# Optimization experiments

Measured on AMD Instinct MI355X. Metric: run time of the kernel, lower is better.

## Reference

```python
import jax, jax.numpy as jnp
import numpy as np

CURRENT_TIME = 1000.0
TIME_WEIGHT = 0.1
NEG_INF = -1e9


def setup_inputs() -> dict:
    key = jax.random.key(0)
    ks = jax.random.split(key, 7)
    B, M, D, C = 1024, 65536, 64, 16
    return {
        "query": jax.random.normal(ks[0], (B, D), dtype=jnp.float32),
        "context": jax.random.normal(ks[1], (B, C), dtype=jnp.float32),
        "mem_keys": jax.random.normal(ks[2], (M, D), dtype=jnp.float32) * 0.1,
        "mem_values": jax.random.normal(ks[3], (M, D), dtype=jnp.float32) * 0.1,
        "mem_contexts": jax.random.normal(ks[4], (M, C), dtype=jnp.float32) * 0.1,
        "mem_timestamps": jax.random.uniform(ks[5], (M, 1), dtype=jnp.float32) * CURRENT_TIME,
        "used_mask": jax.random.randint(ks[6], (M,), 0, 2) > 0,
    }


def reference(query, context, mem_keys, mem_values, mem_contexts, mem_timestamps, used_mask):
    # content score: [B, M]
    scores = jnp.einsum("bd,md->bm", query, mem_keys)
    # context score, scaled by 0.5
    scores = scores + 0.5 * jnp.einsum("bc,mc->bm", context, mem_contexts)
    # time-decay bias, scaled by 0.3 (broadcast over batch)
    decay = jnp.exp(-TIME_WEIGHT * (CURRENT_TIME - mem_timestamps[:, 0]))  # [M]
    scores = scores + 0.3 * decay[None, :]
    # unused slots get -1e9 exactly as torch.full init
    scores = jnp.where(used_mask[None, :], scores, NEG_INF)
    attn = jax.nn.softmax(scores, axis=-1)
    return jnp.einsum("bm,md->bd", attn, mem_values)
```

## Files before the change

### kernel.cpp

```cpp
#include <hip/hip_runtime.h>

typedef float f32x4 __attribute__((ext_vector_type(4)));
typedef __bf16 bf16x8 __attribute__((ext_vector_type(8)));
typedef unsigned int u32;
typedef unsigned short u16;

#define MTOT 65536
#define BTOT 1024
#define DD 64
#define LOG2E 1.44269504088896340736f
#define MFMA __builtin_amdgcn_mfma_f32_16x16x32_bf16

#define NROWBLK ((MTOT + BTOT) * 24 / 256)
#define NVTBLK  (MTOT / 64)
#define ESPACE  (DD * BTOT + BTOT)
#define NSLICE  8

__device__ __forceinline__ u16 f2bf(float f) { return __builtin_bit_cast(u16, (__bf16)f); }
__device__ __forceinline__ u32 pk2(float a, float b) {
    return (u32)f2bf(a) | ((u32)f2bf(b) << 16);
}
__device__ __forceinline__ bf16x8 ldg8(const u16* p) { return *reinterpret_cast<const bf16x8*>(p); }
__device__ __forceinline__ float fexp2(float x) {
#if __has_builtin(__builtin_amdgcn_exp2f)
    return __builtin_amdgcn_exp2f(x);
#else
    return exp2f(x);
#endif
}
__device__ __forceinline__ void glds16(const void* g, void* l) {
    __builtin_amdgcn_global_load_lds((const __attribute__((address_space(1))) u32*)g,
                                     (__attribute__((address_space(3))) u32*)l, 16, 0, 0);
}

__global__ __launch_bounds__(256)
void prep_all(const float* __restrict__ q, const float* __restrict__ ctx,
              const float* __restrict__ K, const float* __restrict__ CT,
              const float* __restrict__ TS, const int* __restrict__ mask,
              const float* __restrict__ V,
              u16* __restrict__ Qc, u16* __restrict__ KC, u16* __restrict__ Vt)
{
    __shared__ u16 L[64][68];
    const int blk = blockIdx.x, t = threadIdx.x;

    if (blk < NROWBLK) {
        const int R = MTOT + BTOT;
        int gid = blk * 256 + t;
        float4 v = {0.f, 0.f, 0.f, 0.f};
        u16* dst;
        if (gid < R * 16) {
            int row = gid >> 4, qd = gid & 15;
            bool isQ = row >= MTOT;
            int r2 = isQ ? row - MTOT : row;
            v = *reinterpret_cast<const float4*>((isQ ? q : K) + (size_t)r2 * 64 + qd * 4);
            if (isQ) { v.x *= LOG2E; v.y *= LOG2E; v.z *= LOG2E; v.w *= LOG2E; }
            dst = (isQ ? Qc : KC) + (size_t)r2 * 96 + qd * 4;
        } else if (gid < R * 20) {
            int i = gid - R * 16;
            int row = i >> 2, qd = i & 3;
            bool isQ = row >= MTOT;
            int r2 = isQ ? row - MTOT : row;
            v = *reinterpret_cast<const float4*>((isQ ? ctx : CT) + (size_t)r2 * 16 + qd * 4);
            if (isQ) { const float s = 0.5f * LOG2E; v.x *= s; v.y *= s; v.z *= s; v.w *= s; }
            dst = (isQ ? Qc : KC) + (size_t)r2 * 96 + 64 + qd * 4;
        } else {
            int i = gid - R * 20;
            int row = i >> 2, qd = i & 3;
            bool isQ = row >= MTOT;
            int r2 = isQ ? row - MTOT : row;
            if (qd == 0)
                v.x = isQ ? LOG2E
                          : (mask[r2] ? 0.3f * __expf(-0.1f * (1000.0f - TS[r2])) : -100.0f);
            dst = (isQ ? Qc : KC) + (size_t)r2 * 96 + 80 + qd * 4;
        }
        ushort4 o = { f2bf(v.x), f2bf(v.y), f2bf(v.z), f2bf(v.w) };
        *reinterpret_cast<ushort4*>(dst) = o;
        return;
    }

    const int m0 = (blk - NROWBLK) * 64;
#pragma unroll
    for (int p = 0; p < 4; ++p) {
        int fi = t + p * 256;
        int mi = fi >> 4, di = (fi & 15) << 2;
        float4 v = *reinterpret_cast<const float4*>(V + (size_t)(m0 + mi) * 64 + di);
        ushort4 o = { f2bf(v.x), f2bf(v.y), f2bf(v.z), f2bf(v.w) };
        *reinterpret_cast<ushort4*>(&L[mi][di]) = o;
    }
    __syncthreads();
    const int d = t >> 2, seg = t & 3;
    u32 pk[8];
#pragma unroll
    for (int pr = 0; pr < 8; ++pr) {
        int c0 = seg * 16 + pr * 2;
        int g32 = c0 >> 5;
        int i0 = c0 & 31, i1 = (c0 + 1) & 31;
        int mp0 = g32 * 32 + (i0 >> 1) + (i0 & 1) * 16;
        int mp1 = g32 * 32 + (i1 >> 1) + (i1 & 1) * 16;
        pk[pr] = (u32)L[mp0][d] | ((u32)L[mp1][d] << 16);
    }
    uint4 A = {pk[0], pk[1], pk[2], pk[3]}, B4 = {pk[4], pk[5], pk[6], pk[7]};
    u16* dst = Vt + (size_t)d * MTOT + m0 + seg * 16;
    *reinterpret_cast<uint4*>(dst)     = A;
    *reinterpret_cast<uint4*>(dst + 8) = B4;
}

__global__ __launch_bounds__(256, 2)
void epmem_mfma(const u16* __restrict__ Qc, const u16* __restrict__ KCg,
                const u16* __restrict__ Vtg,
                float* __restrict__ pl, float* __restrict__ pacc,
                int mper, int NB)
{
    __shared__ __align__(16) u16 KCs[2][64 * 96];
    __shared__ __align__(16) u16 Vts[2][64 * 64];
    __shared__ __align__(16) u16 Pb[4][32][40];

    const int tid = threadIdx.x;
    const int w = tid >> 6, lane = tid & 63;
    const int l15 = lane & 15, g = lane >> 4;

    const int bid = blockIdx.x;
    const int o = (bid & 7) * (NB >> 3) + (bid >> 3);
    const int rt = o & 3, ch = o >> 2;
    const int rbase = rt * 256 + w * 64;

    const u16* qp = Qc + (size_t)(rbase + l15) * 96 + g * 8;
    bf16x8 qf[4][3];
#pragma unroll
    for (int sb = 0; sb < 4; ++sb)
#pragma unroll
        for (int c = 0; c < 3; ++c)
            qf[sb][c] = ldg8(qp + sb * 16 * 96 + c * 32);

    const int m0 = ch * mper;
    const int m1 = (m0 + mper < MTOT) ? (m0 + mper) : MTOT;
    const int ntiles = (m1 > m0) ? ((m1 - m0) >> 6) : 0;

    int kgo[3];
#pragma unroll
    for (int i = 0; i < 3; ++i) {
        int ol = w * 3072 + i * 1024 + lane * 16;
        int row = ol / 192;
        int c = (ol - row * 192) >> 4;
        int u = (c < 8) ? (c ^ (row & 7)) : (8 + ((c & 3) ^ (row & 3)));
        kgo[i] = row * 192 + u * 16;
    }
    int vgo[2];
#pragma unroll
    for (int i = 0; i < 2; ++i) {
        int ol = w * 2048 + i * 1024 + lane * 16;
        int row = ol >> 7, c = (ol >> 4) & 7;
        int u = c ^ (row & 7);
        vgo[i] = row * (MTOT * 2) + u * 16;
    }

    const u32 ow = (l15 == 0) ? 0x3F803F80u : 0u;
    const uint4 ou = {ow, ow, ow, ow};
    const bf16x8 onesf = __builtin_bit_cast(bf16x8, ou);

    f32x4 acc[4][4];
    f32x4 accl[4];
#pragma unroll
    for (int sb = 0; sb < 4; ++sb) {
        accl[sb] = (f32x4){0, 0, 0, 0};
#pragma unroll
        for (int d4 = 0; d4 < 4; ++d4) acc[sb][d4] = (f32x4){0, 0, 0, 0};
    }

    if (ntiles > 0) {
        const char* kb = (const char*)KCg + (size_t)m0 * 192;
        const char* vb = (const char*)Vtg + (size_t)m0 * 2;
#pragma unroll
        for (int i = 0; i < 3; ++i) glds16(kb + kgo[i], (char*)KCs[0] + w * 3072 + i * 1024);
#pragma unroll
        for (int i = 0; i < 2; ++i) glds16(vb + vgo[i], (char*)Vts[0] + w * 2048 + i * 1024);
    }
    __syncthreads();

    char* pbw = (char*)Pb[w];
    const int xr = l15 & 7;
    const int x3 = l15 & 3;

    int cur = 0;
    for (int t = 0; t < ntiles; ++t) {
        if (t + 1 < ntiles) {
            int mt = m0 + ((t + 1) << 6);
            const char* kb = (const char*)KCg + (size_t)mt * 192;
            const char* vb = (const char*)Vtg + (size_t)mt * 2;
            int nb = cur ^ 1;
#pragma unroll
            for (int i = 0; i < 3; ++i) glds16(kb + kgo[i], (char*)KCs[nb] + w * 3072 + i * 1024);
#pragma unroll
            for (int i = 0; i < 2; ++i) glds16(vb + vgo[i], (char*)Vts[nb] + w * 2048 + i * 1024);
        }
        const char* kcb = (const char*)KCs[cur];
        const char* vtb = (const char*)Vts[cur];

#pragma unroll
        for (int j = 0; j < 2; ++j) {
            bf16x8 kf[2][3];
#pragma unroll
            for (int s = 0; s < 2; ++s) {
                int row = j * 32 + s * 16 + l15;
                kf[s][0] = *reinterpret_cast<const bf16x8*>(kcb + row * 192 + (((0 + g) ^ xr) << 4));
                kf[s][1] = *reinterpret_cast<const bf16x8*>(kcb + row * 192 + (((4 + g) ^ xr) << 4));
                kf[s][2] = *reinterpret_cast<const bf16x8*>(kcb + row * 192 + ((8 + (g ^ x3)) << 4));
            }
            bf16x8 vf[4];
#pragma unroll
            for (int d4 = 0; d4 < 4; ++d4) {
                int row = d4 * 16 + l15;
                vf[d4] = *reinterpret_cast<const bf16x8*>(vtb + row * 128 + (((j * 4 + g) ^ xr) << 4));
            }

#pragma unroll
            for (int h = 0; h < 2; ++h) {
                f32x4 S00 = {0,0,0,0}, S01 = {0,0,0,0}, S10 = {0,0,0,0}, S11 = {0,0,0,0};
                S00 = MFMA(qf[2*h][0],   kf[0][0], S00,0,0,0); S00 = MFMA(qf[2*h][1],   kf[0][1], S00,0,0,0); S00 = MFMA(qf[2*h][2],   kf[0][2], S00,0,0,0);
                S01 = MFMA(qf[2*h][0],   kf[1][0], S01,0,0,0); S01 = MFMA(qf[2*h][1],   kf[1][1], S01,0,0,0); S01 = MFMA(qf[2*h][2],   kf[1][2], S01,0,0,0);
                S10 = MFMA(qf[2*h+1][0], kf[0][0], S10,0,0,0); S10 = MFMA(qf[2*h+1][1], kf[0][1], S10,0,0,0); S10 = MFMA(qf[2*h+1][2], kf[0][2], S10,0,0,0);
                S11 = MFMA(qf[2*h+1][0], kf[1][0], S11,0,0,0); S11 = MFMA(qf[2*h+1][1], kf[1][1], S11,0,0,0); S11 = MFMA(qf[2*h+1][2], kf[1][2], S11,0,0,0);

#pragma unroll
                for (int r = 0; r < 4; ++r) {
                    float p00 = fexp2(S00[r]), p01 = fexp2(S01[r]);
                    float p10 = fexp2(S10[r]), p11 = fexp2(S11[r]);
                    int row0 = g * 4 + r, row1 = 16 + g * 4 + r;
                    int cw = (((l15 >> 2) ^ r) << 4) | ((l15 & 3) << 2);
                    *(u32*)(pbw + row0 * 80 + cw) = pk2(p00, p01);
                    *(u32*)(pbw + row1 * 80 + cw) = pk2(p10, p11);
                }
                bf16x8 pa0 = *reinterpret_cast<const bf16x8*>(pbw + l15 * 80        + ((g ^ x3) << 4));
                bf16x8 pa1 = *reinterpret_cast<const bf16x8*>(pbw + (16 + l15) * 80 + ((g ^ x3) << 4));

                acc[2*h][0]   = MFMA(pa0, vf[0], acc[2*h][0],0,0,0);   acc[2*h][1]   = MFMA(pa0, vf[1], acc[2*h][1],0,0,0);
                acc[2*h][2]   = MFMA(pa0, vf[2], acc[2*h][2],0,0,0);   acc[2*h][3]   = MFMA(pa0, vf[3], acc[2*h][3],0,0,0);
                acc[2*h+1][0] = MFMA(pa1, vf[0], acc[2*h+1][0],0,0,0); acc[2*h+1][1] = MFMA(pa1, vf[1], acc[2*h+1][1],0,0,0);
                acc[2*h+1][2] = MFMA(pa1, vf[2], acc[2*h+1][2],0,0,0); acc[2*h+1][3] = MFMA(pa1, vf[3], acc[2*h+1][3],0,0,0);
                accl[2*h]   = MFMA(pa0, onesf, accl[2*h],0,0,0);
                accl[2*h+1] = MFMA(pa1, onesf, accl[2*h+1],0,0,0);
            }
        }
        __syncthreads();
        cur ^= 1;
    }

    if (l15 == 0) {
#pragma unroll
        for (int sb = 0; sb < 4; ++sb)
            *reinterpret_cast<f32x4*>(pl + (size_t)ch * BTOT + rbase + sb * 16 + g * 4) = accl[sb];
    }

    float* bp = pacc + ((size_t)ch * DD + l15) * BTOT + rbase + g * 4;
#pragma unroll
    for (int sb = 0; sb < 4; ++sb)
#pragma unroll
        for (int d4 = 0; d4 < 4; ++d4)
            *reinterpret_cast<f32x4*>(bp + (size_t)(d4 * 16) * BTOT + sb * 16) = acc[sb][d4];
}

__global__ __launch_bounds__(256)
void combineA(const float* __restrict__ pl, const float* __restrict__ pacc,
              float* __restrict__ part, int cper)
{
    int e = blockIdx.x * 256 + threadIdx.x;
    int s = blockIdx.y;
    int c0 = s * cper;
    float v0 = 0.f, v1 = 0.f;
    if (e < DD * BTOT) {
        const float* p = pacc + (size_t)c0 * (DD * BTOT) + e;
#pragma unroll 2
        for (int i = 0; i + 1 < cper; i += 2) {
            v0 += p[(size_t)i * (DD * BTOT)];
            v1 += p[(size_t)(i + 1) * (DD * BTOT)];
        }
        if (cper & 1) v0 += p[(size_t)(cper - 1) * (DD * BTOT)];
    } else {
        const float* p = pl + (size_t)c0 * BTOT + (e - DD * BTOT);
#pragma unroll 2
        for (int i = 0; i + 1 < cper; i += 2) {
            v0 += p[(size_t)i * BTOT];
            v1 += p[(size_t)(i + 1) * BTOT];
        }
        if (cper & 1) v0 += p[(size_t)(cper - 1) * BTOT];
    }
    part[(size_t)s * ESPACE + e] = v0 + v1;
}

__global__ __launch_bounds__(256)
void combineB(const float* __restrict__ part, float* __restrict__ out)
{
    int t = blockIdx.x * 256 + threadIdx.x;
    int d = t >> 10, b = t & 1023;
    float v = 0.f, lssum = 0.f;
#pragma unroll
    for (int s = 0; s < NSLICE; ++s) {
        v     += part[(size_t)s * ESPACE + t];
        lssum += part[(size_t)s * ESPACE + DD * BTOT + b];
    }
    out[(size_t)b * DD + d] = v / lssum;
}

extern "C" void kernel_launch(void* const* d_in, const int* in_sizes, int n_in,
                              void* d_out, int out_size, void* d_ws, size_t ws_size,
                              hipStream_t stream)
{
    const float* q    = (const float*)d_in[0];
    const float* ctx  = (const float*)d_in[1];
    const float* K    = (const float*)d_in[2];
    const float* V    = (const float*)d_in[3];
    const float* CT   = (const float*)d_in[4];
    const float* TS   = (const float*)d_in[5];
    const int*   mask = (const int*)d_in[6];

    char* wsb = (char*)d_ws;
    u16* Qc = (u16*)(wsb);
    u16* KC = (u16*)(wsb + 196608);
    u16* Vt = (u16*)(wsb + 196608 + 12582912);
    size_t fixed = 196608 + 12582912 + 8388608;

    size_t chunk = (size_t)BTOT * (DD + 1) * sizeof(float);
    size_t partB = (size_t)NSLICE * ESPACE * sizeof(float);
    int SPLIT = (int)((ws_size - fixed - partB) / chunk);
    if (SPLIT > 128) SPLIT = 128;
    SPLIT &= ~7;
    if (SPLIT < 8) SPLIT = 8;

    float* pl   = (float*)(wsb + fixed);
    float* pacc = pl + (size_t)SPLIT * BTOT;
    float* part = pacc + (size_t)SPLIT * DD * BTOT;

    int mper = ((MTOT + SPLIT - 1) / SPLIT + 63) & ~63;
    int cper = SPLIT / NSLICE;

    prep_all<<<NROWBLK + NVTBLK, 256, 0, stream>>>(q, ctx, K, CT, TS, mask, V, Qc, KC, Vt);

    int NB = 4 * SPLIT;
    epmem_mfma<<<NB, 256, 0, stream>>>(Qc, KC, Vt, pl, pacc, mper, NB);

    dim3 gA((ESPACE + 255) / 256, NSLICE);
    combineA<<<gA, 256, 0, stream>>>(pl, pacc, part, cper);
    combineB<<<(DD * BTOT) / 256, 256, 0, stream>>>(part, (float*)d_out);
}
```

Measured before the change: 56.01 us.

## Split attention block into eight waves of 32 rows each

The main MFMA kernel now runs 512 threads (8 waves) per block, and each wave handles 32 query rows instead of 64. This halves per-wave query fragments and accumulators, which cuts register pressure and allows higher occupancy (launch bounds 512,4). Only the first four waves issue the async global-to-LDS loads, so the loaded K/V tile is shared by twice as many waves. The cost is more waves contending for LDS reads of K/V fragments, with each wave doing less MFMA work per LDS load.

```diff
diff --git a/kernel.cpp b/kernel.cpp
--- a/kernel.cpp
+++ b/kernel.cpp
@@ -105,7 +105,7 @@
     *reinterpret_cast<uint4*>(dst + 8) = B4;
 }
 
-__global__ __launch_bounds__(256, 2)
+__global__ __launch_bounds__(512, 4)
 void epmem_mfma(const u16* __restrict__ Qc, const u16* __restrict__ KCg,
                 const u16* __restrict__ Vtg,
                 float* __restrict__ pl, float* __restrict__ pacc,
@@ -113,7 +113,7 @@
 {
     __shared__ __align__(16) u16 KCs[2][64 * 96];
     __shared__ __align__(16) u16 Vts[2][64 * 64];
-    __shared__ __align__(16) u16 Pb[4][32][40];
+    __shared__ __align__(16) u16 Pb[8][32][40];
 
     const int tid = threadIdx.x;
     const int w = tid >> 6, lane = tid & 63;
@@ -122,12 +122,12 @@
     const int bid = blockIdx.x;
     const int o = (bid & 7) * (NB >> 3) + (bid >> 3);
     const int rt = o & 3, ch = o >> 2;
-    const int rbase = rt * 256 + w * 64;
+    const int rbase = rt * 256 + w * 32;
 
     const u16* qp = Qc + (size_t)(rbase + l15) * 96 + g * 8;
-    bf16x8 qf[4][3];
-#pragma unroll
-    for (int sb = 0; sb < 4; ++sb)
+    bf16x8 qf[2][3];
+#pragma unroll
+    for (int sb = 0; sb < 2; ++sb)
 #pragma unroll
         for (int c = 0; c < 3; ++c)
             qf[sb][c] = ldg8(qp + sb * 16 * 96 + c * 32);
@@ -136,38 +136,39 @@
     const int m1 = (m0 + mper < MTOT) ? (m0 + mper) : MTOT;
     const int ntiles = (m1 > m0) ? ((m1 - m0) >> 6) : 0;
 
-    int kgo[3];
-#pragma unroll
-    for (int i = 0; i < 3; ++i) {
-        int ol = w * 3072 + i * 1024 + lane * 16;
-        int row = ol / 192;
-        int c = (ol - row * 192) >> 4;
-        int u = (c < 8) ? (c ^ (row & 7)) : (8 + ((c & 3) ^ (row & 3)));
-        kgo[i] = row * 192 + u * 16;
-    }
-    int vgo[2];
-#pragma unroll
-    for (int i = 0; i < 2; ++i) {
-        int ol = w * 2048 + i * 1024 + lane * 16;
-        int row = ol >> 7, c = (ol >> 4) & 7;
-        int u = c ^ (row & 7);
-        vgo[i] = row * (MTOT * 2) + u * 16;
+    int kgo[3], vgo[2];
+    if (w < 4) {
+#pragma unroll
+        for (int i = 0; i < 3; ++i) {
+            int ol = w * 3072 + i * 1024 + lane * 16;
+            int row = ol / 192;
+            int c = (ol - row * 192) >> 4;
+            int u = (c < 8) ? (c ^ (row & 7)) : (8 + ((c & 3) ^ (row & 3)));
+            kgo[i] = row * 192 + u * 16;
+        }
+#pragma unroll
+        for (int i = 0; i < 2; ++i) {
+            int ol = w * 2048 + i * 1024 + lane * 16;
+            int row = ol >> 7, c = (ol >> 4) & 7;
+            int u = c ^ (row & 7);
+            vgo[i] = row * (MTOT * 2) + u * 16;
+        }
     }
 
     const u32 ow = (l15 == 0) ? 0x3F803F80u : 0u;
     const uint4 ou = {ow, ow, ow, ow};
     const bf16x8 onesf = __builtin_bit_cast(bf16x8, ou);
 
-    f32x4 acc[4][4];
-    f32x4 accl[4];
-#pragma unroll
-    for (int sb = 0; sb < 4; ++sb) {
+    f32x4 acc[2][4];
+    f32x4 accl[2];
+#pragma unroll
+    for (int sb = 0; sb < 2; ++sb) {
         accl[sb] = (f32x4){0, 0, 0, 0};
 #pragma unroll
         for (int d4 = 0; d4 < 4; ++d4) acc[sb][d4] = (f32x4){0, 0, 0, 0};
     }
 
-    if (ntiles > 0) {
+    if (ntiles > 0 && w < 4) {
         const char* kb = (const char*)KCg + (size_t)m0 * 192;
         const char* vb = (const char*)Vtg + (size_t)m0 * 2;
 #pragma unroll
@@ -183,7 +184,7 @@
 
     int cur = 0;
     for (int t = 0; t < ntiles; ++t) {
-        if (t + 1 < ntiles) {
+        if (t + 1 < ntiles && w < 4) {
             int mt = m0 + ((t + 1) << 6);
             const char* kb = (const char*)KCg + (size_t)mt * 192;
             const char* vb = (const char*)Vtg + (size_t)mt * 2;
@@ -213,33 +214,30 @@
                 vf[d4] = *reinterpret_cast<const bf16x8*>(vtb + row * 128 + (((j * 4 + g) ^ xr) << 4));
             }
 
-#pragma unroll
-            for (int h = 0; h < 2; ++h) {
-                f32x4 S00 = {0,0,0,0}, S01 = {0,0,0,0}, S10 = {0,0,0,0}, S11 = {0,0,0,0};
-                S00 = MFMA(qf[2*h][0],   kf[0][0], S00,0,0,0); S00 = MFMA(qf[2*h][1],   kf[0][1], S00,0,0,0); S00 = MFMA(qf[2*h][2],   kf[0][2], S00,0,0,0);
-                S01 = MFMA(qf[2*h][0],   kf[1][0], S01,0,0,0); S01 = MFMA(qf[2*h][1],   kf[1][1], S01,0,0,0); S01 = MFMA(qf[2*h][2],   kf[1][2], S01,0,0,0);
-                S10 = MFMA(qf[2*h+1][0], kf[0][0], S10,0,0,0); S10 = MFMA(qf[2*h+1][1], kf[0][1], S10,0,0,0); S10 = MFMA(qf[2*h+1][2], kf[0][2], S10,0,0,0);
-                S11 = MFMA(qf[2*h+1][0], kf[1][0], S11,0,0,0); S11 = MFMA(qf[2*h+1][1], kf[1][1], S11,0,0,0); S11 = MFMA(qf[2*h+1][2], kf[1][2], S11,0,0,0);
-
-#pragma unroll
-                for (int r = 0; r < 4; ++r) {
-                    float p00 = fexp2(S00[r]), p01 = fexp2(S01[r]);
-                    float p10 = fexp2(S10[r]), p11 = fexp2(S11[r]);
-                    int row0 = g * 4 + r, row1 = 16 + g * 4 + r;
-                    int cw = (((l15 >> 2) ^ r) << 4) | ((l15 & 3) << 2);
-                    *(u32*)(pbw + row0 * 80 + cw) = pk2(p00, p01);
-                    *(u32*)(pbw + row1 * 80 + cw) = pk2(p10, p11);
-                }
-                bf16x8 pa0 = *reinterpret_cast<const bf16x8*>(pbw + l15 * 80        + ((g ^ x3) << 4));
-                bf16x8 pa1 = *reinterpret_cast<const bf16x8*>(pbw + (16 + l15) * 80 + ((g ^ x3) << 4));
-
-                acc[2*h][0]   = MFMA(pa0, vf[0], acc[2*h][0],0,0,0);   acc[2*h][1]   = MFMA(pa0, vf[1], acc[2*h][1],0,0,0);
-                acc[2*h][2]   = MFMA(pa0, vf[2], acc[2*h][2],0,0,0);   acc[2*h][3]   = MFMA(pa0, vf[3], acc[2*h][3],0,0,0);
-                acc[2*h+1][0] = MFMA(pa1, vf[0], acc[2*h+1][0],0,0,0); acc[2*h+1][1] = MFMA(pa1, vf[1], acc[2*h+1][1],0,0,0);
-                acc[2*h+1][2] = MFMA(pa1, vf[2], acc[2*h+1][2],0,0,0); acc[2*h+1][3] = MFMA(pa1, vf[3], acc[2*h+1][3],0,0,0);
-                accl[2*h]   = MFMA(pa0, onesf, accl[2*h],0,0,0);
-                accl[2*h+1] = MFMA(pa1, onesf, accl[2*h+1],0,0,0);
+            f32x4 S00 = {0,0,0,0}, S01 = {0,0,0,0}, S10 = {0,0,0,0}, S11 = {0,0,0,0};
+            S00 = MFMA(qf[0][0], kf[0][0], S00,0,0,0); S00 = MFMA(qf[0][1], kf[0][1], S00,0,0,0); S00 = MFMA(qf[0][2], kf[0][2], S00,0,0,0);
+            S01 = MFMA(qf[0][0], kf[1][0], S01,0,0,0); S01 = MFMA(qf[0][1], kf[1][1], S01,0,0,0); S01 = MFMA(qf[0][2], kf[1][2], S01,0,0,0);
+            S10 = MFMA(qf[1][0], kf[0][0], S10,0,0,0); S10 = MFMA(qf[1][1], kf[0][1], S10,0,0,0); S10 = MFMA(qf[1][2], kf[0][2], S10,0,0,0);
+            S11 = MFMA(qf[1][0], kf[1][0], S11,0,0,0); S11 = MFMA(qf[1][1], kf[1][1], S11,0,0,0); S11 = MFMA(qf[1][2], kf[1][2], S11,0,0,0);
+
+#pragma unroll
+            for (int r = 0; r < 4; ++r) {
+                float p00 = fexp2(S00[r]), p01 = fexp2(S01[r]);
+                float p10 = fexp2(S10[r]), p11 = fexp2(S11[r]);
+                int row0 = g * 4 + r, row1 = 16 + g * 4 + r;
+                int cw = (((l15 >> 2) ^ r) << 4) | ((l15 & 3) << 2);
+                *(u32*)(pbw + row0 * 80 + cw) = pk2(p00, p01);
+                *(u32*)(pbw + row1 * 80 + cw) = pk2(p10, p11);
             }
+            bf16x8 pa0 = *reinterpret_cast<const bf16x8*>(pbw + l15 * 80        + ((g ^ x3) << 4));
+            bf16x8 pa1 = *reinterpret_cast<const bf16x8*>(pbw + (16 + l15) * 80 + ((g ^ x3) << 4));
+
+            acc[0][0] = MFMA(pa0, vf[0], acc[0][0],0,0,0); acc[0][1] = MFMA(pa0, vf[1], acc[0][1],0,0,0);
+            acc[0][2] = MFMA(pa0, vf[2], acc[0][2],0,0,0); acc[0][3] = MFMA(pa0, vf[3], acc[0][3],0,0,0);
+            acc[1][0] = MFMA(pa1, vf[0], acc[1][0],0,0,0); acc[1][1] = MFMA(pa1, vf[1], acc[1][1],0,0,0);
+            acc[1][2] = MFMA(pa1, vf[2], acc[1][2],0,0,0); acc[1][3] = MFMA(pa1, vf[3], acc[1][3],0,0,0);
+            accl[0] = MFMA(pa0, onesf, accl[0],0,0,0);
+            accl[1] = MFMA(pa1, onesf, accl[1],0,0,0);
         }
         __syncthreads();
         cur ^= 1;
@@ -247,13 +245,13 @@
 
     if (l15 == 0) {
 #pragma unroll
-        for (int sb = 0; sb < 4; ++sb)
+        for (int sb = 0; sb < 2; ++sb)
             *reinterpret_cast<f32x4*>(pl + (size_t)ch * BTOT + rbase + sb * 16 + g * 4) = accl[sb];
     }
 
     float* bp = pacc + ((size_t)ch * DD + l15) * BTOT + rbase + g * 4;
 #pragma unroll
-    for (int sb = 0; sb < 4; ++sb)
+    for (int sb = 0; sb < 2; ++sb)
 #pragma unroll
         for (int d4 = 0; d4 < 4; ++d4)
             *reinterpret_cast<f32x4*>(bp + (size_t)(d4 * 16) * BTOT + sb * 16) = acc[sb][d4];
@@ -336,7 +334,7 @@
     prep_all<<<NROWBLK + NVTBLK, 256, 0, stream>>>(q, ctx, K, CT, TS, mask, V, Qc, KC, Vt);
 
     int NB = 4 * SPLIT;
-    epmem_mfma<<<NB, 256, 0, stream>>>(Qc, KC, Vt, pl, pacc, mper, NB);
+    epmem_mfma<<<NB, 512, 0, stream>>>(Qc, KC, Vt, pl, pacc, mper, NB);
 
     dim3 gA((ESPACE + 255) / 256, NSLICE);
     combineA<<<gA, 256, 0, stream>>>(pl, pacc, part, cper);
```

Result: no change. 55.55 us (-0.8%).
